# Performance work log

Hardware: AMD Instinct MI355X
Metric: run time of the kernel (lower is better)

Reference implementation:

```python
import jax, jax.numpy as jnp
import numpy as np

N_NODES = 20000
STEPS = 10  # message_passing_steps


def _mlp(x, p):
    # 3-layer MLP: Linear->ReLU->Linear->ReLU->Linear (no final activation)
    W1, b1, W2, b2, W3, b3 = p
    h = jax.nn.relu(x @ W1 + b1)
    h = jax.nn.relu(h @ W2 + b2)
    return h @ W3 + b3


def _aggregate(dst, edge_attr, num_nodes):
    # scatter_add of edge features into destination nodes, degree-normalized (deg clamped to >=1)
    agg = jax.ops.segment_sum(edge_attr, dst, num_segments=num_nodes)
    deg = jax.ops.segment_sum(jnp.ones((dst.shape[0], 1), edge_attr.dtype), dst, num_segments=num_nodes)
    return agg / jnp.maximum(deg, 1.0)


def setup_inputs() -> dict:
    key = jax.random.key(0)
    N, EM, EC = N_NODES, 120000, 20000
    ND, MD, CD, OD, L = 12, 7, 4, 3, 128
    keys = iter(jax.random.split(key, 128))

    def lin(i, o):
        return (jax.random.normal(next(keys), (i, o), jnp.float32) * 0.05,
                jax.random.normal(next(keys), (o,), jnp.float32) * 0.05)

    inp = {
        "node_x": jax.random.normal(next(keys), (N, ND), jnp.float32),
        "mesh_edge_attr": jax.random.normal(next(keys), (EM, MD), jnp.float32),
        "contact_edge_attr": jax.random.normal(next(keys), (EC, CD), jnp.float32),
    }
    dims = {"ne": (ND, L), "me": (MD, L), "ce": (CD, L), "pe": (3 * L, L), "pn": (3 * L, L), "de": (L, OD)}
    for name, (i, o) in dims.items():
        W1, b1 = lin(i, L)
        W2, b2 = lin(L, L)
        W3, b3 = lin(L, o)
        for pn, p in zip(["W1", "b1", "W2", "b2", "W3", "b3"], [W1, b1, W2, b2, W3, b3]):
            inp[name + "_" + pn] = p
    inp["mesh_edge_index"] = jax.random.randint(next(keys), (2, EM), 0, N)
    inp["contact_edge_index"] = jax.random.randint(next(keys), (2, EC), 0, N)
    return inp


def reference(node_x, mesh_edge_attr, contact_edge_attr,
              ne_W1, ne_b1, ne_W2, ne_b2, ne_W3, ne_b3,
              me_W1, me_b1, me_W2, me_b2, me_W3, me_b3,
              ce_W1, ce_b1, ce_W2, ce_b2, ce_W3, ce_b3,
              pe_W1, pe_b1, pe_W2, pe_b2, pe_W3, pe_b3,
              pn_W1, pn_b1, pn_W2, pn_b2, pn_W3, pn_b3,
              de_W1, de_b1, de_W2, de_b2, de_W3, de_b3,
              mesh_edge_index, contact_edge_index):
    ne = (ne_W1, ne_b1, ne_W2, ne_b2, ne_W3, ne_b3)
    mep = (me_W1, me_b1, me_W2, me_b2, me_W3, me_b3)
    cep = (ce_W1, ce_b1, ce_W2, ce_b2, ce_W3, ce_b3)
    pe = (pe_W1, pe_b1, pe_W2, pe_b2, pe_W3, pe_b3)
    pn = (pn_W1, pn_b1, pn_W2, pn_b2, pn_W3, pn_b3)
    de = (de_W1, de_b1, de_W2, de_b2, de_W3, de_b3)
    N = node_x.shape[0]
    # encode
    x = _mlp(node_x, ne)                 # [N, 128]
    me = _mlp(mesh_edge_attr, mep)       # [EM, 128]
    ce = _mlp(contact_edge_attr, cep)    # [EC, 128]
    msrc, mdst = mesh_edge_index[0], mesh_edge_index[1]
    csrc, cdst = contact_edge_index[0], contact_edge_index[1]
    # process (shared edge_mlp for both edge types, residual updates)
    for _ in range(STEPS):
        me = me + _mlp(jnp.concatenate([x[msrc], x[mdst], me], axis=-1), pe)
        ce = ce + _mlp(jnp.concatenate([x[csrc], x[cdst], ce], axis=-1), pe)
        agg_m = _aggregate(mdst, me, N)
        agg_c = _aggregate(cdst, ce, N)
        x = x + _mlp(jnp.concatenate([x, agg_m, agg_c], axis=-1), pn)
    # decode
    return _mlp(x, de)                   # [N, 3]
```

## Files before the change

### kernel.cpp

```cpp
#include <hip/hip_runtime.h>
#include <stdint.h>

typedef unsigned short u16;
typedef __attribute__((ext_vector_type(8))) short bf16x8;
typedef __attribute__((ext_vector_type(4))) float f32x4;

#define NNODES 20000
#define EM 120000
#define EC 20000
#define LDIM 128
#define MT 32
#define MT2 64
#define A_STR 392
#define H_STR 136
#define D_STR 132

__device__ __forceinline__ u16 f2bf(float f){
  uint32_t b = __float_as_uint(f);
  b += 0x7FFF + ((b >> 16) & 1);
  return (u16)(b >> 16);
}

__device__ __forceinline__ f32x4 mfma16(bf16x8 a, bf16x8 b, f32x4 c){
  return __builtin_amdgcn_mfma_f32_16x16x32_bf16(a, b, c, 0, 0, 0);
}

template<int KB>
__device__ __forceinline__ void layer(const u16* sIn, int in_str, const u16* Wp,
                                      int wr, int wc, int lane, f32x4 acc[4]){
  const int row = wr*16 + (lane & 15);
  const int kg  = lane >> 4;
  #pragma unroll
  for (int kb = 0; kb < KB; ++kb){
    bf16x8 a = *(const bf16x8*)(sIn + row*in_str + kb*32 + kg*8);
    const u16* wb = Wp + (((kb*8 + wc*4)*64 + lane) << 3);
    #pragma unroll
    for (int nf = 0; nf < 4; ++nf){
      bf16x8 b = *(const bf16x8*)(wb + (nf << 9));
      acc[nf] = mfma16(a, b, acc[nf]);
    }
  }
}

__device__ __forceinline__ void hid_epi(f32x4 acc[4], const float* bias,
                                        int wr, int wc, int lane, u16* sOut){
  const int cl = lane & 15;
  const int r0 = wr*16 + (lane >> 4)*4;
  #pragma unroll
  for (int nf = 0; nf < 4; ++nf){
    int col = wc*64 + nf*16 + cl;
    float bv = bias[col];
    #pragma unroll
    for (int r = 0; r < 4; ++r){
      float v = acc[nf][r] + bv;
      sOut[(r0 + r)*H_STR + col] = f2bf(v > 0.f ? v : 0.f);
    }
  }
}

__device__ __forceinline__ void zero4(f32x4 acc[4]){
  const f32x4 vz = {0.f, 0.f, 0.f, 0.f};
  #pragma unroll
  for (int i = 0; i < 4; ++i) acc[i] = vz;
}

template<int KB, int STR>
__device__ __forceinline__ void layer64(const u16* sIn, const u16* Wp,
                                        int wr, int wc, int lane, f32x4 acc[2][2]){
  const int r0 = wr*32 + (lane & 15);
  const int kg = lane >> 4;
  const u16* a0p = sIn + r0*STR + kg*8;
  const u16* a1p = a0p + 16*STR;
  const u16* wb  = Wp + (((wc*2)*64 + lane) << 3);
  #pragma unroll
  for (int kb = 0; kb < KB; ++kb){
    bf16x8 a0 = *(const bf16x8*)(a0p + kb*32);
    bf16x8 a1 = *(const bf16x8*)(a1p + kb*32);
    const u16* wk = wb + kb*4096;
    bf16x8 b0 = *(const bf16x8*)(wk);
    bf16x8 b1 = *(const bf16x8*)(wk + 512);
    acc[0][0] = mfma16(a0, b0, acc[0][0]);
    acc[1][0] = mfma16(a1, b0, acc[1][0]);
    acc[0][1] = mfma16(a0, b1, acc[0][1]);
    acc[1][1] = mfma16(a1, b1, acc[1][1]);
  }
}

template<int STR>
__device__ __forceinline__ void hid_epi64(f32x4 acc[2][2], const float* bias,
                                          int wr, int wc, int lane, u16* sOut){
  const int cl = lane & 15;
  const int rq = (lane >> 4)*4;
  #pragma unroll
  for (int rf = 0; rf < 2; ++rf){
    int r0 = wr*32 + rf*16 + rq;
    #pragma unroll
    for (int nf = 0; nf < 2; ++nf){
      int col = wc*32 + nf*16 + cl;
      float bv = bias[col];
      #pragma unroll
      for (int r = 0; r < 4; ++r){
        float v = acc[rf][nf][r] + bv;
        sOut[(r0 + r)*STR + col] = f2bf(v > 0.f ? v : 0.f);
      }
    }
  }
}

__device__ __forceinline__ void zero22(f32x4 acc[2][2]){
  const f32x4 vz = {0.f, 0.f, 0.f, 0.f};
  acc[0][0] = vz; acc[0][1] = vz; acc[1][0] = vz; acc[1][1] = vz;
}

template<int KB, int STR>
__device__ __forceinline__ void layer32(const u16* sIn, const u16* Wp,
                                        int wr, int wc, int lane, f32x4 acc[2]){
  const int r0 = wr*16 + (lane & 15);
  const int kg = lane >> 4;
  const u16* a0p = sIn + r0*STR + kg*8;
  const u16* wb  = Wp + (((wc*2)*64 + lane) << 3);
  #pragma unroll
  for (int kb = 0; kb < KB; ++kb){
    bf16x8 a0 = *(const bf16x8*)(a0p + kb*32);
    const u16* wk = wb + kb*4096;
    bf16x8 b0 = *(const bf16x8*)(wk);
    bf16x8 b1 = *(const bf16x8*)(wk + 512);
    acc[0] = mfma16(a0, b0, acc[0]);
    acc[1] = mfma16(a0, b1, acc[1]);
  }
}

template<int STR>
__device__ __forceinline__ void hid_epi32(f32x4 acc[2], const float* bias,
                                          int wr, int wc, int lane, u16* sOut){
  const int cl = lane & 15;
  const int r0 = wr*16 + (lane >> 4)*4;
  #pragma unroll
  for (int nf = 0; nf < 2; ++nf){
    int col = wc*32 + nf*16 + cl;
    float bv = bias[col];
    #pragma unroll
    for (int r = 0; r < 4; ++r){
      float v = acc[nf][r] + bv;
      sOut[(r0 + r)*STR + col] = f2bf(v > 0.f ? v : 0.f);
    }
  }
}

struct PackDesc { const float* src; int K_raw, N_raw, NF, elem_off; };
struct PackArgs { PackDesc d[18]; int total; };

__global__ __launch_bounds__(256) void pack_weights(PackArgs pa, u16* dst){
  int idx = blockIdx.x*256 + threadIdx.x;
  if (idx >= pa.total) return;
  int di = 0;
  #pragma unroll
  for (int i = 1; i < 18; ++i) if (idx >= pa.d[i].elem_off) di = i;
  PackDesc dd = pa.d[di];
  int e = idx - dd.elem_off;
  int f = e >> 9, lane = (e >> 3) & 63, j = e & 7;
  int kb = f / dd.NF, nf = f % dd.NF;
  int k = kb*32 + (lane >> 4)*8 + j;
  int n = nf*16 + (lane & 15);
  float v = (k < dd.K_raw && n < dd.N_raw) ? dd.src[k*dd.N_raw + n] : 0.f;
  dst[idx] = f2bf(v);
}

__global__ __launch_bounds__(256) void hist_kernel(const int* mdst, const int* cdst,
                                                   int* cnt_m, int* cnt_c){
  int i = blockIdx.x*256 + threadIdx.x;
  if (i < EM) atomicAdd(&cnt_m[mdst[i]], 1);
  else if (i < EM + EC) atomicAdd(&cnt_c[cdst[i - EM]], 1);
}

struct ScanArgs { const int *cnt_m, *cnt_c; int *start_m, *start_c, *cur_m, *cur_c; };

__global__ __launch_bounds__(256) void scan_kernel(ScanArgs a){
  const int n = NNODES;
  const int* cnt = blockIdx.x == 0 ? a.cnt_m : a.cnt_c;
  int* start     = blockIdx.x == 0 ? a.start_m : a.start_c;
  int* cur       = blockIdx.x == 0 ? a.cur_m : a.cur_c;
  __shared__ int part[256];
  __shared__ int base[257];
  int t = threadIdx.x;
  const int per = (n + 255) / 256;
  int lo = t*per, hi = min(n, lo + per);
  int s = 0;
  for (int j = lo; j < hi; ++j) s += cnt[j];
  part[t] = s;
  __syncthreads();
  if (t == 0){
    int run = 0;
    for (int i = 0; i < 256; ++i){ base[i] = run; run += part[i]; }
    base[256] = run;
  }
  __syncthreads();
  int run = base[t];
  for (int j = lo; j < hi; ++j){ start[j] = run; cur[j] = run; run += cnt[j]; }
  if (t == 255) start[n] = base[256];
}

__global__ __launch_bounds__(256) void scatter_kernel(const int* mdst, const int* cdst,
                                                      int* cur_m, int* cur_c,
                                                      int* pos_m, int* pos_c){
  int i = blockIdx.x*256 + threadIdx.x;
  if (i < EM){
    int p = atomicAdd(&cur_m[mdst[i]], 1);
    pos_m[i] = p;
  } else if (i < EM + EC){
    int e = i - EM;
    int p = atomicAdd(&cur_c[cdst[e]], 1);
    pos_c[e] = p;
  }
}

__global__ __launch_bounds__(256) void permsd_kernel(const int* msrc, const int* mdst, const int* pos_m,
                                                     const int* csrc, const int* cdst, const int* pos_c,
                                                     int* sp_m, int* dp_m, int* sp_c, int* dp_c){
  int i = blockIdx.x*256 + threadIdx.x;
  if (i < EM){
    int p = pos_m[i];
    sp_m[p] = msrc[i]; dp_m[p] = mdst[i];
  } else if (i < EM + EC){
    int e = i - EM;
    int p = pos_c[e];
    sp_c[p] = csrc[e]; dp_c[p] = cdst[e];
  }
}

struct EncArgs {
  const float* in; int Kraw;
  const u16 *Wp1, *Wp2, *Wp3;
  const float *b1, *b2, *b3;
  float* out_f32; u16* out_b16;
  const int* perm;
};

__global__ __launch_bounds__(256) void enc_kernel(EncArgs a){
  __shared__ u16 sA[MT*A_STR];
  __shared__ u16 sH[MT*H_STR];
  const int tid = threadIdx.x, lane = tid & 63, w = tid >> 6, wr = w & 1, wc = w >> 1;
  const int m0 = blockIdx.x * MT;
  for (int i = tid; i < MT*32; i += 256){
    int row = i >> 5, c = i & 31;
    float v = (c < a.Kraw) ? a.in[(size_t)(m0 + row)*a.Kraw + c] : 0.f;
    sA[row*A_STR + c] = f2bf(v);
  }
  __syncthreads();
  f32x4 acc[4]; zero4(acc);
  layer<1>(sA, A_STR, a.Wp1, wr, wc, lane, acc);
  hid_epi(acc, a.b1, wr, wc, lane, sH);
  __syncthreads();
  zero4(acc);
  layer<4>(sH, H_STR, a.Wp2, wr, wc, lane, acc);
  hid_epi(acc, a.b2, wr, wc, lane, sA);
  __syncthreads();
  zero4(acc);
  layer<4>(sA, H_STR, a.Wp3, wr, wc, lane, acc);
  const int cl = lane & 15, r0l = wr*16 + (lane >> 4)*4;
  #pragma unroll
  for (int nf = 0; nf < 4; ++nf){
    int col = wc*64 + nf*16 + cl;
    float bv = a.b3[col];
    #pragma unroll
    for (int r = 0; r < 4; ++r){
      int m = m0 + r0l + r;
      int om = a.perm ? a.perm[m] : m;
      float v = acc[nf][r] + bv;
      a.out_f32[(size_t)om*LDIM + col] = v;
      if (a.out_b16) a.out_b16[(size_t)om*LDIM + col] = f2bf(v);
    }
  }
}

struct EdgeArgs {
  const u16 *Wp1, *Wp2, *Wp3;
  const float *b1, *b2, *b3;
  const u16* x_b16;
  const int *sp_m, *dp_m, *sp_c, *dp_c;
  float *me_f32, *ce_f32;
  int mesh_blocks;
};

__global__ __launch_bounds__(512, 6) void edge_kernel(EdgeArgs a){
  __shared__ u16 sCat[MT2*A_STR];
  const int tid = threadIdx.x, lane = tid & 63, w = tid >> 6, wr = w & 1, wc = w >> 1;
  const bool mesh = (int)blockIdx.x < a.mesh_blocks;
  const int e0 = (mesh ? (int)blockIdx.x : (int)blockIdx.x - a.mesh_blocks) * MT2;
  const int E = mesh ? EM : EC;
  const int* sp = mesh ? a.sp_m : a.sp_c;
  const int* dp = mesh ? a.dp_m : a.dp_c;
  float* ff = mesh ? a.me_f32 : a.ce_f32;

  #pragma unroll
  for (int i = tid; i < MT2*32; i += 512){
    int row = i >> 5, c = i & 31;
    int e = e0 + row; if (e >= E) e = E - 1;
    const u16* xp = (c < 16) ? a.x_b16 + (size_t)sp[e]*LDIM + c*8
                             : a.x_b16 + (size_t)dp[e]*LDIM + (c-16)*8;
    *(bf16x8*)(sCat + row*A_STR + c*8) = *(const bf16x8*)xp;
  }
  const int srow = tid >> 3, sj = tid & 7;
  int se = e0 + srow; if (se >= E) se = E - 1;
  const f32x4* fp = (const f32x4*)(ff + (size_t)se*LDIM + sj*16);
  f32x4 p0 = fp[0], p1 = fp[1], p2 = fp[2], p3 = fp[3];
  {
    bf16x8 t0, t1;
    #pragma unroll
    for (int k = 0; k < 4; ++k){
      t0[k] = (short)f2bf(p0[k]); t0[k+4] = (short)f2bf(p1[k]);
      t1[k] = (short)f2bf(p2[k]); t1[k+4] = (short)f2bf(p3[k]);
    }
    *(bf16x8*)(sCat + srow*A_STR + 256 + sj*16) = t0;
    *(bf16x8*)(sCat + srow*A_STR + 256 + sj*16 + 8) = t1;
  }
  __syncthreads();

  f32x4 acc[2][2]; zero22(acc);
  layer64<12, A_STR>(sCat, a.Wp1, wr, wc, lane, acc);
  __syncthreads();
  hid_epi64<A_STR>(acc, a.b1, wr, wc, lane, sCat + 256);
  __syncthreads();
  zero22(acc);
  layer64<4, A_STR>(sCat + 256, a.Wp2, wr, wc, lane, acc);
  hid_epi64<A_STR>(acc, a.b2, wr, wc, lane, sCat);
  __syncthreads();
  zero22(acc);
  layer64<4, A_STR>(sCat, a.Wp3, wr, wc, lane, acc);
  __syncthreads();

  float* dd = (float*)sCat;
  {
    const int cl = lane & 15, rq = (lane >> 4)*4;
    #pragma unroll
    for (int rf = 0; rf < 2; ++rf){
      #pragma unroll
      for (int nf = 0; nf < 2; ++nf){
        int col = wc*32 + nf*16 + cl;
        float bv = a.b3[col];
        #pragma unroll
        for (int r = 0; r < 4; ++r)
          dd[(wr*32 + rf*16 + rq + r)*D_STR + col] = acc[rf][nf][r] + bv;
      }
    }
  }
  __syncthreads();
  if (e0 + srow < E){
    float* op = ff + (size_t)(e0 + srow)*LDIM + sj*16;
    const f32x4* dp_ = (const f32x4*)(dd + srow*D_STR + sj*16);
    f32x4 n0 = p0 + dp_[0], n1 = p1 + dp_[1], n2 = p2 + dp_[2], n3 = p3 + dp_[3];
    ((f32x4*)op)[0] = n0; ((f32x4*)op)[1] = n1; ((f32x4*)op)[2] = n2; ((f32x4*)op)[3] = n3;
  }
}

struct NodeArgs {
  const u16 *Wp1, *Wp2, *Wp3;
  const float *b1, *b2, *b3;
  const u16* x_b16_in;
  const float *me_f32, *ce_f32;
  const int *start_m, *start_c;
  float* x_f32; u16* x_b16_out;
};

__global__ __launch_bounds__(512, 6) void node_kernel(NodeArgs a){
  __shared__ u16 sA[MT*A_STR];
  const int tid = threadIdx.x, lane = tid & 63, w = tid >> 6, wr = w & 1, wc = w >> 1;
  const int n0 = blockIdx.x * MT;

  {
    int row = tid >> 4, ch = tid & 15;
    *(bf16x8*)(sA + row*A_STR + ch*8) =
        *(const bf16x8*)(a.x_b16_in + (size_t)(n0+row)*LDIM + ch*8);
  }
  {
    const int r = tid >> 4, c0 = (tid & 15) * 8;
    const int n = n0 + r;
    {
      int s = a.start_m[n], e = a.start_m[n+1];
      f32x4 a0{0,0,0,0}, a1{0,0,0,0};
      for (int j = s; j < e; ++j){
        const f32x4* p = (const f32x4*)(a.me_f32 + (size_t)j*LDIM + c0);
        a0 += p[0]; a1 += p[1];
      }
      float inv = 1.f / fmaxf((float)(e - s), 1.f);
      bf16x8 t;
      #pragma unroll
      for (int k = 0; k < 4; ++k){ t[k] = (short)f2bf(a0[k]*inv); t[k+4] = (short)f2bf(a1[k]*inv); }
      *(bf16x8*)(sA + r*A_STR + 128 + c0) = t;
    }
    {
      int s = a.start_c[n], e = a.start_c[n+1];
      f32x4 a0{0,0,0,0}, a1{0,0,0,0};
      for (int j = s; j < e; ++j){
        const f32x4* p = (const f32x4*)(a.ce_f32 + (size_t)j*LDIM + c0);
        a0 += p[0]; a1 += p[1];
      }
      float inv = 1.f / fmaxf((float)(e - s), 1.f);
      bf16x8 t;
      #pragma unroll
      for (int k = 0; k < 4; ++k){ t[k] = (short)f2bf(a0[k]*inv); t[k+4] = (short)f2bf(a1[k]*inv); }
      *(bf16x8*)(sA + r*A_STR + 256 + c0) = t;
    }
  }
  __syncthreads();

  f32x4 acc[2]; acc[0] = f32x4{0,0,0,0}; acc[1] = f32x4{0,0,0,0};
  layer32<12, A_STR>(sA, a.Wp1, wr, wc, lane, acc);
  __syncthreads();
  hid_epi32<A_STR>(acc, a.b1, wr, wc, lane, sA + 256);
  __syncthreads();
  acc[0] = f32x4{0,0,0,0}; acc[1] = f32x4{0,0,0,0};
  layer32<4, A_STR>(sA + 256, a.Wp2, wr, wc, lane, acc);
  hid_epi32<A_STR>(acc, a.b2, wr, wc, lane, sA);
  __syncthreads();
  acc[0] = f32x4{0,0,0,0}; acc[1] = f32x4{0,0,0,0};
  layer32<4, A_STR>(sA, a.Wp3, wr, wc, lane, acc);

  const int cl = lane & 15, rq = (lane >> 4)*4;
  #pragma unroll
  for (int r = 0; r < 4; ++r){
    int n = n0 + wr*16 + rq + r;
    #pragma unroll
    for (int nf = 0; nf < 2; ++nf){
      int col = wc*32 + nf*16 + cl;
      float nv = a.x_f32[(size_t)n*LDIM + col] + acc[nf][r] + a.b3[col];
      a.x_f32[(size_t)n*LDIM + col] = nv;
      a.x_b16_out[(size_t)n*LDIM + col] = f2bf(nv);
    }
  }
}

struct DecArgs {
  const u16 *Wp1, *Wp2, *Wp3;
  const float *b1, *b2, *b3;
  const u16* x_b16; float* out;
};

__global__ __launch_bounds__(256) void dec_kernel(DecArgs a){
  __shared__ u16 sA[MT*A_STR];
  __shared__ u16 sH[MT*H_STR];
  const int tid = threadIdx.x, lane = tid & 63, w = tid >> 6, wr = w & 1, wc = w >> 1;
  const int n0 = blockIdx.x * MT;
  for (int i = tid; i < MT*16; i += 256){
    int row = i >> 4, ch = i & 15;
    *(bf16x8*)(sA + row*H_STR + ch*8) = *(const bf16x8*)(a.x_b16 + (size_t)(n0+row)*LDIM + ch*8);
  }
  __syncthreads();
  f32x4 acc[4]; zero4(acc);
  layer<4>(sA, H_STR, a.Wp1, wr, wc, lane, acc);
  hid_epi(acc, a.b1, wr, wc, lane, sH);
  __syncthreads();
  zero4(acc);
  layer<4>(sH, H_STR, a.Wp2, wr, wc, lane, acc);
  hid_epi(acc, a.b2, wr, wc, lane, sA);
  __syncthreads();
  if (wc == 0){
    f32x4 a3 = {0.f, 0.f, 0.f, 0.f};
    const int row = wr*16 + (lane & 15), kg = lane >> 4;
    #pragma unroll
    for (int kb = 0; kb < 4; ++kb){
      bf16x8 av = *(const bf16x8*)(sA + row*H_STR + kb*32 + kg*8);
      bf16x8 bv = *(const bf16x8*)(a.Wp3 + ((kb*64 + lane) << 3));
      a3 = mfma16(av, bv, a3);
    }
    const int cl = lane & 15, r0l = wr*16 + (lane >> 4)*4;
    if (cl < 3){
      #pragma unroll
      for (int r = 0; r < 4; ++r)
        a.out[(size_t)(n0 + r0l + r)*3 + cl] = a3[r] + a.b3[cl];
    }
  }
}

extern "C" void kernel_launch(void* const* d_in, const int* in_sizes, int n_in,
                              void* d_out, int out_size, void* d_ws, size_t ws_size,
                              hipStream_t stream){
  auto F = [&](int i){ return (const float*)d_in[i]; };
  const float* node_x   = F(0);
  const float* mesh_attr = F(1);
  const float* cont_attr = F(2);
  const int* mei = (const int*)d_in[39];
  const int* cei = (const int*)d_in[40];
  const int *msrc = mei, *mdst = mei + EM, *csrc = cei, *cdst = cei + EC;

  char* ws = (char*)d_ws;
  size_t off = 0;
  auto take = [&](size_t b)->void*{ void* p = ws + off; off += (b + 255) & ~(size_t)255; return p; };
  float* x_f32  = (float*)take((size_t)NNODES*LDIM*4);
  u16*   x_b16  = (u16*)  take((size_t)NNODES*LDIM*2);
  float* me_f32 = (float*)take((size_t)EM*LDIM*4);
  float* ce_f32 = (float*)take((size_t)EC*LDIM*4);
  u16*   wpack  = (u16*)  take((size_t)309248*2);
  int* cnt_m   = (int*)take((size_t)NNODES*4);
  int* cnt_c   = (int*)take((size_t)NNODES*4);
  int* start_m = (int*)take((size_t)(NNODES+1)*4);
  int* start_c = (int*)take((size_t)(NNODES+1)*4);
  int* cur_m   = (int*)take((size_t)NNODES*4);
  int* cur_c   = (int*)take((size_t)NNODES*4);
  int* pos_m   = (int*)take((size_t)EM*4);
  int* pos_c   = (int*)take((size_t)EC*4);
  int* sp_m    = (int*)take((size_t)EM*4);
  int* dp_m    = (int*)take((size_t)EM*4);
  int* sp_c    = (int*)take((size_t)EC*4);
  int* dp_c    = (int*)take((size_t)EC*4);

  static const int tbl[18][5] = {
    {3,12,128,32,128},{5,128,128,128,128},{7,128,128,128,128},
    {9,7,128,32,128},{11,128,128,128,128},{13,128,128,128,128},
    {15,4,128,32,128},{17,128,128,128,128},{19,128,128,128,128},
    {21,384,128,384,128},{23,128,128,128,128},{25,128,128,128,128},
    {27,384,128,384,128},{29,128,128,128,128},{31,128,128,128,128},
    {33,128,128,128,128},{35,128,128,128,128},{37,128,3,128,16}};
  PackArgs pa; int eo = 0; int offs[18];
  for (int i = 0; i < 18; ++i){
    offs[i] = eo;
    pa.d[i].src = F(tbl[i][0]);
    pa.d[i].K_raw = tbl[i][1];
    pa.d[i].N_raw = tbl[i][2];
    pa.d[i].NF = tbl[i][4] / 16;
    pa.d[i].elem_off = eo;
    eo += tbl[i][3] * tbl[i][4];
  }
  pa.total = eo;
  pack_weights<<<dim3(eo/256), dim3(256), 0, stream>>>(pa, wpack);

  size_t cnt_span = ((char*)cnt_c - (char*)cnt_m) + (size_t)NNODES*4;
  hipMemsetAsync(cnt_m, 0, cnt_span, stream);
  hist_kernel<<<dim3((EM + EC + 255)/256), dim3(256), 0, stream>>>(mdst, cdst, cnt_m, cnt_c);
  ScanArgs sa{cnt_m, cnt_c, start_m, start_c, cur_m, cur_c};
  scan_kernel<<<dim3(2), dim3(256), 0, stream>>>(sa);
  scatter_kernel<<<dim3((EM + EC + 255)/256), dim3(256), 0, stream>>>(mdst, cdst, cur_m, cur_c, pos_m, pos_c);
  permsd_kernel<<<dim3((EM + EC + 255)/256), dim3(256), 0, stream>>>(msrc, mdst, pos_m, csrc, cdst, pos_c,
                                                                     sp_m, dp_m, sp_c, dp_c);

  EncArgs en{node_x, 12, wpack+offs[0], wpack+offs[1], wpack+offs[2], F(4), F(6), F(8), x_f32, x_b16, nullptr};
  enc_kernel<<<dim3(NNODES/MT), dim3(256), 0, stream>>>(en);
  EncArgs em{mesh_attr, 7, wpack+offs[3], wpack+offs[4], wpack+offs[5], F(10), F(12), F(14), me_f32, nullptr, pos_m};
  enc_kernel<<<dim3(EM/MT), dim3(256), 0, stream>>>(em);
  EncArgs ec{cont_attr, 4, wpack+offs[6], wpack+offs[7], wpack+offs[8], F(16), F(18), F(20), ce_f32, nullptr, pos_c};
  enc_kernel<<<dim3(EC/MT), dim3(256), 0, stream>>>(ec);

  EdgeArgs ea;
  ea.Wp1 = wpack+offs[9]; ea.Wp2 = wpack+offs[10]; ea.Wp3 = wpack+offs[11];
  ea.b1 = F(22); ea.b2 = F(24); ea.b3 = F(26);
  ea.x_b16 = x_b16;
  ea.sp_m = sp_m; ea.dp_m = dp_m; ea.sp_c = sp_c; ea.dp_c = dp_c;
  ea.me_f32 = me_f32; ea.ce_f32 = ce_f32;
  ea.mesh_blocks = EM/MT2;

  NodeArgs na;
  na.Wp1 = wpack+offs[12]; na.Wp2 = wpack+offs[13]; na.Wp3 = wpack+offs[14];
  na.b1 = F(28); na.b2 = F(30); na.b3 = F(32);
  na.x_b16_in = x_b16;
  na.me_f32 = me_f32; na.ce_f32 = ce_f32;
  na.start_m = start_m; na.start_c = start_c;
  na.x_f32 = x_f32; na.x_b16_out = x_b16;

  const int edge_blocks = EM/MT2 + (EC + MT2 - 1)/MT2;
  const int node_blocks = NNODES/MT;
  for (int s = 0; s < 10; ++s){
    edge_kernel<<<dim3(edge_blocks), dim3(512), 0, stream>>>(ea);
    node_kernel<<<dim3(node_blocks), dim3(512), 0, stream>>>(na);
  }

  DecArgs da{wpack+offs[15], wpack+offs[16], wpack+offs[17], F(34), F(36), F(38), x_b16, (float*)d_out};
  dec_kernel<<<dim3(NNODES/MT), dim3(256), 0, stream>>>(da);
}
```

Baseline: 1.150 ms.

## Split edge first-layer K loop to shrink shared tile; unroll CSR aggregation

The edge kernel's first MLP layer now runs in two phases. The gathered x[src]/x[dst] tile (K=256) is multiplied first, then the same shared buffer is reused for the bf16 edge features (K=128). This cuts the shared-memory row stride from 392 to 264 elements, which can allow more resident blocks per CU, at the cost of an extra barrier. Separately, the node kernel's CSR segment-sum loops are unrolled by two so more independent loads are in flight.

```diff
diff --git a/kernel.cpp b/kernel.cpp
--- a/kernel.cpp
+++ b/kernel.cpp
@@ -12,6 +12,7 @@
 #define MT 32
 #define MT2 64
 #define A_STR 392
+#define X_STR 264
 #define H_STR 136
 #define D_STR 132
 
@@ -283,7 +284,7 @@
 };
 
 __global__ __launch_bounds__(512, 6) void edge_kernel(EdgeArgs a){
-  __shared__ u16 sCat[MT2*A_STR];
+  __shared__ u16 sCat[MT2*X_STR];
   const int tid = threadIdx.x, lane = tid & 63, w = tid >> 6, wr = w & 1, wc = w >> 1;
   const bool mesh = (int)blockIdx.x < a.mesh_blocks;
   const int e0 = (mesh ? (int)blockIdx.x : (int)blockIdx.x - a.mesh_blocks) * MT2;
@@ -292,18 +293,25 @@
   const int* dp = mesh ? a.dp_m : a.dp_c;
   float* ff = mesh ? a.me_f32 : a.ce_f32;
 
+  const int srow = tid >> 3, sj = tid & 7;
+  int se = e0 + srow; if (se >= E) se = E - 1;
+  const f32x4* fp = (const f32x4*)(ff + (size_t)se*LDIM + sj*16);
+  f32x4 p0 = fp[0], p1 = fp[1], p2 = fp[2], p3 = fp[3];
+
   #pragma unroll
   for (int i = tid; i < MT2*32; i += 512){
     int row = i >> 5, c = i & 31;
     int e = e0 + row; if (e >= E) e = E - 1;
     const u16* xp = (c < 16) ? a.x_b16 + (size_t)sp[e]*LDIM + c*8
                              : a.x_b16 + (size_t)dp[e]*LDIM + (c-16)*8;
-    *(bf16x8*)(sCat + row*A_STR + c*8) = *(const bf16x8*)xp;
-  }
-  const int srow = tid >> 3, sj = tid & 7;
-  int se = e0 + srow; if (se >= E) se = E - 1;
-  const f32x4* fp = (const f32x4*)(ff + (size_t)se*LDIM + sj*16);
-  f32x4 p0 = fp[0], p1 = fp[1], p2 = fp[2], p3 = fp[3];
+    *(bf16x8*)(sCat + row*X_STR + c*8) = *(const bf16x8*)xp;
+  }
+  __syncthreads();
+
+  f32x4 acc[2][2]; zero22(acc);
+  layer64<8, X_STR>(sCat, a.Wp1, wr, wc, lane, acc);
+  __syncthreads();
+
   {
     bf16x8 t0, t1;
     #pragma unroll
@@ -311,22 +319,20 @@
       t0[k] = (short)f2bf(p0[k]); t0[k+4] = (short)f2bf(p1[k]);
       t1[k] = (short)f2bf(p2[k]); t1[k+4] = (short)f2bf(p3[k]);
     }
-    *(bf16x8*)(sCat + srow*A_STR + 256 + sj*16) = t0;
-    *(bf16x8*)(sCat + srow*A_STR + 256 + sj*16 + 8) = t1;
-  }
-  __syncthreads();
-
-  f32x4 acc[2][2]; zero22(acc);
-  layer64<12, A_STR>(sCat, a.Wp1, wr, wc, lane, acc);
-  __syncthreads();
-  hid_epi64<A_STR>(acc, a.b1, wr, wc, lane, sCat + 256);
+    *(bf16x8*)(sCat + srow*X_STR + sj*16) = t0;
+    *(bf16x8*)(sCat + srow*X_STR + sj*16 + 8) = t1;
+  }
+  __syncthreads();
+
+  layer64<4, X_STR>(sCat, a.Wp1 + 8*4096, wr, wc, lane, acc);
+  hid_epi64<X_STR>(acc, a.b1, wr, wc, lane, sCat + 128);
   __syncthreads();
   zero22(acc);
-  layer64<4, A_STR>(sCat + 256, a.Wp2, wr, wc, lane, acc);
-  hid_epi64<A_STR>(acc, a.b2, wr, wc, lane, sCat);
+  layer64<4, X_STR>(sCat + 128, a.Wp2, wr, wc, lane, acc);
+  hid_epi64<X_STR>(acc, a.b2, wr, wc, lane, sCat);
   __syncthreads();
   zero22(acc);
-  layer64<4, A_STR>(sCat, a.Wp3, wr, wc, lane, acc);
+  layer64<4, X_STR>(sCat, a.Wp3, wr, wc, lane, acc);
   __syncthreads();
 
   float* dd = (float*)sCat;
@@ -378,7 +384,15 @@
     {
       int s = a.start_m[n], e = a.start_m[n+1];
       f32x4 a0{0,0,0,0}, a1{0,0,0,0};
-      for (int j = s; j < e; ++j){
+      int j = s;
+      for (; j + 1 < e; j += 2){
+        const f32x4* pA = (const f32x4*)(a.me_f32 + (size_t)j*LDIM + c0);
+        const f32x4* pB = (const f32x4*)(a.me_f32 + (size_t)(j+1)*LDIM + c0);
+        f32x4 qA0 = pA[0], qA1 = pA[1], qB0 = pB[0], qB1 = pB[1];
+        a0 += qA0; a1 += qA1;
+        a0 += qB0; a1 += qB1;
+      }
+      if (j < e){
         const f32x4* p = (const f32x4*)(a.me_f32 + (size_t)j*LDIM + c0);
         a0 += p[0]; a1 += p[1];
       }
@@ -391,7 +405,15 @@
     {
       int s = a.start_c[n], e = a.start_c[n+1];
       f32x4 a0{0,0,0,0}, a1{0,0,0,0};
-      for (int j = s; j < e; ++j){
+      int j = s;
+      for (; j + 1 < e; j += 2){
+        const f32x4* pA = (const f32x4*)(a.ce_f32 + (size_t)j*LDIM + c0);
+        const f32x4* pB = (const f32x4*)(a.ce_f32 + (size_t)(j+1)*LDIM + c0);
+        f32x4 qA0 = pA[0], qA1 = pA[1], qB0 = pB[0], qB1 = pB[1];
+        a0 += qA0; a1 += qA1;
+        a0 += qB0; a1 += qB1;
+      }
+      if (j < e){
         const f32x4* p = (const f32x4*)(a.ce_f32 + (size_t)j*LDIM + c0);
         a0 += p[0]; a1 += p[1];
       }
```

Result: no change. 1.150 ms (-0.0%).
